# Kernel tuning notes

Measured on AMD Instinct MI355X. Metric: run time of the kernel, lower is better.

Reference implementation:

```python
import jax, jax.numpy as jnp
import numpy as np

B, N, NODE_DIM, HID, HEAD = 32, 1024, 14, 64, 128
EDGE_PROB = 0.01


def setup_inputs() -> dict:
    key = jax.random.key(0)
    ks = jax.random.split(key, 12)
    x = jax.random.normal(ks[0], (B, N, NODE_DIM), dtype=jnp.float32)
    # sparse binary adjacency with self-loops (matches eye + edge scatter)
    adj = (jax.random.uniform(ks[1], (B, N, N)) < EDGE_PROB).astype(jnp.float32)
    adjacency = jnp.maximum(adj, jnp.eye(N, dtype=jnp.float32)[None])
    def lin(k, din, dout):
        kw, kb = jax.random.split(k)
        w = jax.random.normal(kw, (din, dout), dtype=jnp.float32) / np.sqrt(din)
        b = jnp.zeros((dout,), dtype=jnp.float32)
        return w, b
    W1, b1 = lin(ks[2], NODE_DIM, HID)
    W2, b2 = lin(ks[3], HID, HID)
    W3, b3 = lin(ks[4], HID, HID)
    Wf1, bf1 = lin(ks[5], HID, HEAD)
    Wf2, bf2 = lin(ks[6], HEAD, 1)
    return {"x": x, "adjacency": adjacency, "W1": W1, "b1": b1, "W2": W2,
            "b2": b2, "W3": W3, "b3": b3, "Wf1": Wf1, "bf1": bf1,
            "Wf2": Wf2, "bf2": bf2}


def _dense_graph_conv(x, norm_adj, W, b):
    # (D^-1/2 A D^-1/2) @ x, then linear
    return jnp.einsum('bnm,bmd->bnd', norm_adj, x) @ W + b


def reference(x, adjacency, W1, b1, W2, b2, W3, b3, Wf1, bf1, Wf2, bf2):
    degree = adjacency.sum(axis=-1)                      # [B,N]
    d_inv_sqrt = jnp.clip(degree, 1.0, None) ** -0.5
    norm_adj = d_inv_sqrt[..., :, None] * adjacency * d_inv_sqrt[..., None, :]
    h = jax.nn.relu(_dense_graph_conv(x, norm_adj, W1, b1))
    h = jax.nn.relu(_dense_graph_conv(h, norm_adj, W2, b2))
    h = jax.nn.relu(_dense_graph_conv(h, norm_adj, W3, b3))
    pooled = h.mean(axis=1)                              # [B,HID]
    return jax.nn.relu(pooled @ Wf1 + bf1) @ Wf2 + bf2   # [B,1]
```

## Files before the change

### kernel.cpp

```cpp
#include <hip/hip_runtime.h>
#include <math.h>

#define NN 1024
#define HID 64
#define HEADD 128
#define NODE_DIM 14
#define BATCH 32
#define CAP 64
#define ROWS (BATCH * NN)
#define RPW 8

__device__ __forceinline__ int swz4(int blk, int wv) {
    int x = blk & 7, q = blk >> 3;
    int batch = x + 8 * (q >> 8);
    return batch * NN + ((q & 255) << 2) + wv;
}
__device__ __forceinline__ int swz32(int blk, int wv) {
    int x = blk & 7, q = blk >> 3;
    int batch = x + 8 * (q >> 5);
    return batch * NN + ((q & 31) << 5) + wv * RPW;
}

__device__ __forceinline__ float rl_f(float v, int k) {
    return __int_as_float(__builtin_amdgcn_readlane(__float_as_int(v), k));
}

__global__ __launch_bounds__(256) void k_build(const float* __restrict__ adj,
                                               const float* __restrict__ x,
                                               const float* __restrict__ W1,
                                               unsigned short* __restrict__ csr,
                                               int* __restrict__ nnz_g,
                                               float* __restrict__ dinv,
                                               float* __restrict__ g1,
                                               float* __restrict__ pooled) {
    __shared__ float sW1[NODE_DIM * HID];
    for (int i = threadIdx.x; i < NODE_DIM * HID; i += 256) sW1[i] = W1[i];
    if (blockIdx.x < 8) pooled[blockIdx.x * 256 + threadIdx.x] = 0.f;
    int wv = threadIdx.x >> 6, lane = threadIdx.x & 63;
    int row = swz4(blockIdx.x, wv);
    const float4* rp = reinterpret_cast<const float4*>(adj + (size_t)row * NN);
    unsigned long long lt = ((unsigned long long)1 << lane) - 1;
    int base = 0;
#pragma unroll
    for (int j = 0; j < 4; ++j) {
        float4 v = rp[lane + 64 * j];
        float vv[4] = {v.x, v.y, v.z, v.w};
#pragma unroll
        for (int k = 0; k < 4; ++k) {
            unsigned long long mk = __ballot(vv[k] != 0.0f);
            if (mk) {
                if (vv[k] != 0.0f) {
                    int pos = base + __popcll(mk & lt);
                    if (pos < CAP)
                        csr[row * CAP + pos] = (unsigned short)((lane + 64 * j) * 4 + k);
                }
                base += __popcll(mk);
            }
        }
    }
    if (lane == 0) {
        nnz_g[row] = base < CAP ? base : CAP;
        dinv[row] = 1.0f / sqrtf((float)(base < 1 ? 1 : base));
    }
    __syncthreads();
    float acc = 0.f;
    const float* xr = x + (size_t)row * NODE_DIM;
#pragma unroll
    for (int d = 0; d < NODE_DIM; ++d) acc += xr[d] * sW1[d * HID + lane];
    g1[(size_t)row * HID + lane] = acc;
}

__device__ __forceinline__ void spmm8(const float* __restrict__ g_in,
                                      int bbase, const int n[RPW],
                                      const int idx[RPW], const float dv[RPW],
                                      int lane, float acc[RPW]) {
    int nmax = 0;
#pragma unroll
    for (int r = 0; r < RPW; ++r) { acc[r] = 0.f; nmax = n[r] > nmax ? n[r] : nmax; }
    for (int k = 0; k < nmax; ++k) {
        float w[RPW], v[RPW];
#pragma unroll
        for (int r = 0; r < RPW; ++r) {
            int j = __builtin_amdgcn_readlane(idx[r], k);
            w[r] = rl_f(dv[r], k);
            v[r] = g_in[(bbase + j) * HID + lane];
        }
#pragma unroll
        for (int r = 0; r < RPW; ++r) acc[r] += w[r] * v[r];
    }
}

__global__ __launch_bounds__(256, 4) void k_layer(const float* __restrict__ g_in,
                                                  const unsigned short* __restrict__ csr,
                                                  const int* __restrict__ nnz_g,
                                                  const float* __restrict__ dinv,
                                                  const float* __restrict__ bias,
                                                  const float* __restrict__ W,
                                                  float* __restrict__ g_out) {
    int wv = threadIdx.x >> 6, lane = threadIdx.x & 63;
    float wreg[HID];
#pragma unroll
    for (int d = 0; d < HID; ++d) wreg[d] = W[d * HID + lane];
    int row0 = swz32(blockIdx.x, wv);
    int bbase = row0 & ~(NN - 1);
    float bb = bias[lane];
    int n[RPW], idx[RPW];
    float dv[RPW];
#pragma unroll
    for (int r = 0; r < RPW; ++r) {
        int row = row0 + r;
        n[r] = __builtin_amdgcn_readfirstlane(nnz_g[row]);
        idx[r] = (lane < n[r]) ? (int)csr[row * CAP + lane] : 0;
        dv[r] = (lane < n[r]) ? dinv[bbase + idx[r]] : 0.f;
    }
    float acc[RPW];
    spmm8(g_in, bbase, n, idx, dv, lane, acc);
    float h[RPW];
#pragma unroll
    for (int r = 0; r < RPW; ++r)
        h[r] = fmaxf(dinv[row0 + r] * acc[r] + bb, 0.f);
    float o[RPW];
#pragma unroll
    for (int r = 0; r < RPW; ++r) o[r] = 0.f;
#pragma unroll
    for (int d = 0; d < HID; ++d) {
        float w = wreg[d];
#pragma unroll
        for (int r = 0; r < RPW; ++r) o[r] += rl_f(h[r], d) * w;
    }
#pragma unroll
    for (int r = 0; r < RPW; ++r)
        g_out[(size_t)(row0 + r) * HID + lane] = o[r];
}

__global__ __launch_bounds__(256, 4) void k_layer3(const float* __restrict__ g_in,
                                                   const unsigned short* __restrict__ csr,
                                                   const int* __restrict__ nnz_g,
                                                   const float* __restrict__ dinv,
                                                   const float* __restrict__ bias,
                                                   float* __restrict__ pooled) {
    __shared__ float sred[4][HID];
    int wv = threadIdx.x >> 6, lane = threadIdx.x & 63;
    int row0 = swz32(blockIdx.x, wv);
    int bbase = row0 & ~(NN - 1);
    float bb = bias[lane];
    int n[RPW], idx[RPW];
    float dv[RPW];
#pragma unroll
    for (int r = 0; r < RPW; ++r) {
        int row = row0 + r;
        n[r] = __builtin_amdgcn_readfirstlane(nnz_g[row]);
        idx[r] = (lane < n[r]) ? (int)csr[row * CAP + lane] : 0;
        dv[r] = (lane < n[r]) ? dinv[bbase + idx[r]] : 0.f;
    }
    float acc[RPW];
    spmm8(g_in, bbase, n, idx, dv, lane, acc);
    float s = 0.f;
#pragma unroll
    for (int r = 0; r < RPW; ++r)
        s += fmaxf(dinv[row0 + r] * acc[r] + bb, 0.f);
    sred[wv][lane] = s;
    __syncthreads();
    if (wv == 0) {
        float tot = sred[0][lane] + sred[1][lane] + sred[2][lane] + sred[3][lane];
        atomicAdd(&pooled[(bbase >> 10) * HID + lane], tot);
    }
}

__global__ __launch_bounds__(128) void k_head(const float* __restrict__ pooled_sum,
                                              const float* __restrict__ Wf1,
                                              const float* __restrict__ bf1,
                                              const float* __restrict__ Wf2,
                                              const float* __restrict__ bf2,
                                              float* __restrict__ out) {
    int b = blockIdx.x, t = threadIdx.x;
    __shared__ float p[HID];
    __shared__ float hid[HEADD];
    if (t < HID) p[t] = pooled_sum[b * HID + t] * (1.0f / NN);
    __syncthreads();
    float acc = bf1[t];
    for (int d = 0; d < HID; ++d) acc += p[d] * Wf1[d * HEADD + t];
    hid[t] = fmaxf(acc, 0.f);
    __syncthreads();
    if (t < 64) {
        float v = hid[t] * Wf2[t] + hid[t + 64] * Wf2[t + 64];
#pragma unroll
        for (int off = 32; off > 0; off >>= 1) v += __shfl_down(v, off, 64);
        if (t == 0) out[b] = v + bf2[0];
    }
}

extern "C" void kernel_launch(void* const* d_in, const int* in_sizes, int n_in,
                              void* d_out, int out_size, void* d_ws, size_t ws_size,
                              hipStream_t stream) {
    const float* x   = (const float*)d_in[0];
    const float* adj = (const float*)d_in[1];
    const float* W1  = (const float*)d_in[2];
    const float* b1  = (const float*)d_in[3];
    const float* W2  = (const float*)d_in[4];
    const float* b2  = (const float*)d_in[5];
    const float* W3  = (const float*)d_in[6];
    const float* b3  = (const float*)d_in[7];
    const float* Wf1 = (const float*)d_in[8];
    const float* bf1 = (const float*)d_in[9];
    const float* Wf2 = (const float*)d_in[10];
    const float* bf2 = (const float*)d_in[11];
    float* out = (float*)d_out;

    char* ws = (char*)d_ws;
    size_t off = 0;
    unsigned short* csr = (unsigned short*)(ws + off); off += (size_t)ROWS * CAP * 2;
    int*   nnz_g  = (int*)(ws + off);   off += (size_t)ROWS * 4;
    float* dinv   = (float*)(ws + off); off += (size_t)ROWS * 4;
    float* pooled = (float*)(ws + off); off += 4096 * 4;
    float* g1     = (float*)(ws + off); off += (size_t)ROWS * HID * 4;
    float* g2     = (float*)(ws + off); off += (size_t)ROWS * HID * 4;
    float* g3     = (float*)(ws + off);

    k_build <<<ROWS / 4, 256, 0, stream>>>(adj, x, W1, csr, nnz_g, dinv, g1, pooled);
    k_layer <<<ROWS / 32, 256, 0, stream>>>(g1, csr, nnz_g, dinv, b1, W2, g2);
    k_layer <<<ROWS / 32, 256, 0, stream>>>(g2, csr, nnz_g, dinv, b2, W3, g3);
    k_layer3<<<ROWS / 32, 256, 0, stream>>>(g3, csr, nnz_g, dinv, b3, pooled);
    k_head  <<<BATCH, 128, 0, stream>>>(pooled, Wf1, bf1, Wf2, bf2, out);
}
```

Measured before the change: 293.2 us.

## Fold degree normalization into features and pipeline the sparse gather loop

The source-node D^-1/2 scaling is folded into each layer's output (and into the layer-1 input), so the SpMM becomes a plain sum of gathered rows with no per-edge weight gather or readlane. The CSR now stores batch-global node indices, and padding lanes point at a zeroed extra row, which removes index arithmetic from the inner loop. The gather loop is software-pipelined with one iteration of prefetch. W is staged in LDS instead of 64 registers per lane, which allows an occupancy target of 6. This trades register pressure for LDS reads in the dense matmul and adds one barrier per block.

New measurement: 277.6 us. 1.06x faster.

```diff
diff --git a/kernel.cpp b/kernel.cpp
--- a/kernel.cpp
+++ b/kernel.cpp
@@ -8,6 +8,8 @@
 #define BATCH 32
 #define CAP 64
 #define ROWS (BATCH * NN)
+#define ZROW ROWS
+#define GROW (ROWS + 16)
 #define RPW 8
 
 __device__ __forceinline__ int swz4(int blk, int wv) {
@@ -23,6 +25,9 @@
 
 __device__ __forceinline__ float rl_f(float v, int k) {
     return __int_as_float(__builtin_amdgcn_readlane(__float_as_int(v), k));
+}
+__device__ __forceinline__ float rfl_f(float v) {
+    return __int_as_float(__builtin_amdgcn_readfirstlane(__float_as_int(v)));
 }
 
 __global__ __launch_bounds__(256) void k_build(const float* __restrict__ adj,
@@ -32,12 +37,21 @@
                                                int* __restrict__ nnz_g,
                                                float* __restrict__ dinv,
                                                float* __restrict__ g1,
+                                               float* __restrict__ g2,
+                                               float* __restrict__ g3,
                                                float* __restrict__ pooled) {
     __shared__ float sW1[NODE_DIM * HID];
     for (int i = threadIdx.x; i < NODE_DIM * HID; i += 256) sW1[i] = W1[i];
     if (blockIdx.x < 8) pooled[blockIdx.x * 256 + threadIdx.x] = 0.f;
+    if (blockIdx.x == 8 && threadIdx.x < 64) {
+        int t = threadIdx.x;
+        g1[(size_t)ZROW * HID + t] = 0.f;
+        g2[(size_t)ZROW * HID + t] = 0.f;
+        g3[(size_t)ZROW * HID + t] = 0.f;
+    }
     int wv = threadIdx.x >> 6, lane = threadIdx.x & 63;
     int row = swz4(blockIdx.x, wv);
+    int brow = row & ~(NN - 1);
     const float4* rp = reinterpret_cast<const float4*>(adj + (size_t)row * NN);
     unsigned long long lt = ((unsigned long long)1 << lane) - 1;
     int base = 0;
@@ -52,79 +66,90 @@
                 if (vv[k] != 0.0f) {
                     int pos = base + __popcll(mk & lt);
                     if (pos < CAP)
-                        csr[row * CAP + pos] = (unsigned short)((lane + 64 * j) * 4 + k);
+                        csr[row * CAP + pos] =
+                            (unsigned short)(brow + (lane + 64 * j) * 4 + k);
                 }
                 base += __popcll(mk);
             }
         }
     }
+    float di = 1.0f / sqrtf((float)(base < 1 ? 1 : base));
     if (lane == 0) {
         nnz_g[row] = base < CAP ? base : CAP;
-        dinv[row] = 1.0f / sqrtf((float)(base < 1 ? 1 : base));
+        dinv[row] = di;
     }
     __syncthreads();
     float acc = 0.f;
     const float* xr = x + (size_t)row * NODE_DIM;
 #pragma unroll
     for (int d = 0; d < NODE_DIM; ++d) acc += xr[d] * sW1[d * HID + lane];
-    g1[(size_t)row * HID + lane] = acc;
+    g1[(size_t)row * HID + lane] = acc * di;
 }
 
 __device__ __forceinline__ void spmm8(const float* __restrict__ g_in,
-                                      int bbase, const int n[RPW],
-                                      const int idx[RPW], const float dv[RPW],
+                                      const int n[RPW], const int idx[RPW],
                                       int lane, float acc[RPW]) {
-    int nmax = 0;
+    int nmax = 1;
 #pragma unroll
     for (int r = 0; r < RPW; ++r) { acc[r] = 0.f; nmax = n[r] > nmax ? n[r] : nmax; }
-    for (int k = 0; k < nmax; ++k) {
-        float w[RPW], v[RPW];
+    float v[RPW];
+#pragma unroll
+    for (int r = 0; r < RPW; ++r) {
+        int j = __builtin_amdgcn_readlane(idx[r], 0);
+        v[r] = g_in[(size_t)j * HID + lane];
+    }
+    for (int k = 1; k < nmax; ++k) {
+        float vn[RPW];
 #pragma unroll
         for (int r = 0; r < RPW; ++r) {
             int j = __builtin_amdgcn_readlane(idx[r], k);
-            w[r] = rl_f(dv[r], k);
-            v[r] = g_in[(bbase + j) * HID + lane];
+            vn[r] = g_in[(size_t)j * HID + lane];
         }
 #pragma unroll
-        for (int r = 0; r < RPW; ++r) acc[r] += w[r] * v[r];
-    }
-}
-
-__global__ __launch_bounds__(256, 4) void k_layer(const float* __restrict__ g_in,
+        for (int r = 0; r < RPW; ++r) { acc[r] += v[r]; v[r] = vn[r]; }
+    }
+#pragma unroll
+    for (int r = 0; r < RPW; ++r) acc[r] += v[r];
+}
+
+__global__ __launch_bounds__(256, 6) void k_layer(const float* __restrict__ g_in,
                                                   const unsigned short* __restrict__ csr,
                                                   const int* __restrict__ nnz_g,
                                                   const float* __restrict__ dinv,
                                                   const float* __restrict__ bias,
                                                   const float* __restrict__ W,
                                                   float* __restrict__ g_out) {
+    __shared__ float sW[HID * HID];
+    {
+        const float4* Wv = reinterpret_cast<const float4*>(W);
+        float4* sWv = reinterpret_cast<float4*>(sW);
+        for (int i = threadIdx.x; i < HID * HID / 4; i += 256) sWv[i] = Wv[i];
+    }
     int wv = threadIdx.x >> 6, lane = threadIdx.x & 63;
-    float wreg[HID];
-#pragma unroll
-    for (int d = 0; d < HID; ++d) wreg[d] = W[d * HID + lane];
     int row0 = swz32(blockIdx.x, wv);
-    int bbase = row0 & ~(NN - 1);
     float bb = bias[lane];
     int n[RPW], idx[RPW];
-    float dv[RPW];
+    float dr[RPW];
 #pragma unroll
     for (int r = 0; r < RPW; ++r) {
         int row = row0 + r;
         n[r] = __builtin_amdgcn_readfirstlane(nnz_g[row]);
-        idx[r] = (lane < n[r]) ? (int)csr[row * CAP + lane] : 0;
-        dv[r] = (lane < n[r]) ? dinv[bbase + idx[r]] : 0.f;
+        idx[r] = (lane < n[r]) ? (int)csr[row * CAP + lane] : ZROW;
+        dr[r] = rfl_f(dinv[row]);
     }
     float acc[RPW];
-    spmm8(g_in, bbase, n, idx, dv, lane, acc);
+    spmm8(g_in, n, idx, lane, acc);
     float h[RPW];
 #pragma unroll
     for (int r = 0; r < RPW; ++r)
-        h[r] = fmaxf(dinv[row0 + r] * acc[r] + bb, 0.f);
+        h[r] = fmaxf(dr[r] * acc[r] + bb, 0.f) * dr[r];
+    __syncthreads();
     float o[RPW];
 #pragma unroll
     for (int r = 0; r < RPW; ++r) o[r] = 0.f;
 #pragma unroll
     for (int d = 0; d < HID; ++d) {
-        float w = wreg[d];
+        float w = sW[d * HID + lane];
 #pragma unroll
         for (int r = 0; r < RPW; ++r) o[r] += rl_f(h[r], d) * w;
     }
@@ -133,7 +158,7 @@
         g_out[(size_t)(row0 + r) * HID + lane] = o[r];
 }
 
-__global__ __launch_bounds__(256, 4) void k_layer3(const float* __restrict__ g_in,
+__global__ __launch_bounds__(256, 6) void k_layer3(const float* __restrict__ g_in,
                                                    const unsigned short* __restrict__ csr,
                                                    const int* __restrict__ nnz_g,
                                                    const float* __restrict__ dinv,
@@ -142,28 +167,27 @@
     __shared__ float sred[4][HID];
     int wv = threadIdx.x >> 6, lane = threadIdx.x & 63;
     int row0 = swz32(blockIdx.x, wv);
-    int bbase = row0 & ~(NN - 1);
     float bb = bias[lane];
     int n[RPW], idx[RPW];
-    float dv[RPW];
+    float dr[RPW];
 #pragma unroll
     for (int r = 0; r < RPW; ++r) {
         int row = row0 + r;
         n[r] = __builtin_amdgcn_readfirstlane(nnz_g[row]);
-        idx[r] = (lane < n[r]) ? (int)csr[row * CAP + lane] : 0;
-        dv[r] = (lane < n[r]) ? dinv[bbase + idx[r]] : 0.f;
+        idx[r] = (lane < n[r]) ? (int)csr[row * CAP + lane] : ZROW;
+        dr[r] = rfl_f(dinv[row]);
     }
     float acc[RPW];
-    spmm8(g_in, bbase, n, idx, dv, lane, acc);
+    spmm8(g_in, n, idx, lane, acc);
     float s = 0.f;
 #pragma unroll
     for (int r = 0; r < RPW; ++r)
-        s += fmaxf(dinv[row0 + r] * acc[r] + bb, 0.f);
+        s += fmaxf(dr[r] * acc[r] + bb, 0.f);
     sred[wv][lane] = s;
     __syncthreads();
     if (wv == 0) {
         float tot = sred[0][lane] + sred[1][lane] + sred[2][lane] + sred[3][lane];
-        atomicAdd(&pooled[(bbase >> 10) * HID + lane], tot);
+        atomicAdd(&pooled[(row0 >> 10) * HID + lane], tot);
     }
 }
 
@@ -213,11 +237,11 @@
     int*   nnz_g  = (int*)(ws + off);   off += (size_t)ROWS * 4;
     float* dinv   = (float*)(ws + off); off += (size_t)ROWS * 4;
     float* pooled = (float*)(ws + off); off += 4096 * 4;
-    float* g1     = (float*)(ws + off); off += (size_t)ROWS * HID * 4;
-    float* g2     = (float*)(ws + off); off += (size_t)ROWS * HID * 4;
+    float* g1     = (float*)(ws + off); off += (size_t)GROW * HID * 4;
+    float* g2     = (float*)(ws + off); off += (size_t)GROW * HID * 4;
     float* g3     = (float*)(ws + off);
 
-    k_build <<<ROWS / 4, 256, 0, stream>>>(adj, x, W1, csr, nnz_g, dinv, g1, pooled);
+    k_build <<<ROWS / 4, 256, 0, stream>>>(adj, x, W1, csr, nnz_g, dinv, g1, g2, g3, pooled);
     k_layer <<<ROWS / 32, 256, 0, stream>>>(g1, csr, nnz_g, dinv, b1, W2, g2);
     k_layer <<<ROWS / 32, 256, 0, stream>>>(g2, csr, nnz_g, dinv, b2, W3, g3);
     k_layer3<<<ROWS / 32, 256, 0, stream>>>(g3, csr, nnz_g, dinv, b3, pooled);
```
